# Optimization experiments

Measured on AMD Instinct MI355X. Metric: run time of the kernel, lower is better.

## Reference

```python
import jax, jax.numpy as jnp
import numpy as np

B, A, D, H = 2048, 32, 128, 256

def setup_inputs() -> dict:
    key = jax.random.key(0)
    ks = jax.random.split(key, 12)
    s = lambda fan_in: 1.0 / np.sqrt(fan_in)
    return {
        "obs": jax.random.normal(ks[0], (B, A, D), dtype=jnp.float32),
        "act": jax.random.normal(ks[1], (B, A, 8), dtype=jnp.float32),
        "enc_W": jax.random.uniform(ks[2], (H, D), jnp.float32, -s(D), s(D)),
        "enc_b": jax.random.uniform(ks[3], (H,), jnp.float32, -s(D), s(D)),
        "fobs_W": jax.random.uniform(ks[4], (H, H), jnp.float32, -s(H), s(H)),
        "fobs_b": jax.random.uniform(ks[5], (H,), jnp.float32, -s(H), s(H)),
        "W_ih": jax.random.uniform(ks[6], (3 * H, H), jnp.float32, -s(H), s(H)),
        "b_ih": jax.random.uniform(ks[7], (3 * H,), jnp.float32, -s(H), s(H)),
        "W_hh": jax.random.uniform(ks[8], (3 * H, H), jnp.float32, -s(H), s(H)),
        "b_hh": jax.random.uniform(ks[9], (3 * H,), jnp.float32, -s(H), s(H)),
        "dec_W": jax.random.uniform(ks[10], (1, H), jnp.float32, -s(H), s(H)),
        "dec_b": jax.random.uniform(ks[11], (1,), jnp.float32, -s(H), s(H)),
    }

def _gru_cell(x, h, W_ih, b_ih, W_hh, b_hh):
    # torch.nn.GRUCell: gates stacked as [reset, update, new]
    gi = x @ W_ih.T + b_ih          # [N, 3H]
    gh = h @ W_hh.T + b_hh          # [N, 3H]
    i_r, i_z, i_n = jnp.split(gi, 3, axis=-1)
    h_r, h_z, h_n = jnp.split(gh, 3, axis=-1)
    r = jax.nn.sigmoid(i_r + h_r)
    z = jax.nn.sigmoid(i_z + h_z)
    n = jnp.tanh(i_n + r * h_n)
    return (1.0 - z) * n + z * h

def reference(obs, act, enc_W, enc_b, fobs_W, fobs_b, W_ih, b_ih, W_hh, b_hh, dec_W, dec_b):
    b, a, d = obs.shape
    x = obs.reshape(b * a, d)                         # [B*A, D]
    e = jax.nn.relu(x @ enc_W.T + enc_b)              # encoder + ReLU
    h = e @ fobs_W.T + fobs_b                         # h_out
    # k = 0: comm input is zeros
    h = _gru_cell(jnp.zeros_like(h), h, W_ih, b_ih, W_hh, b_hh)
    # k = 1: masked mean over other agents == (sum_j h_j - h_i) / n_agents
    hA = h.reshape(b, a, -1)                          # [B, A, H]
    c = (hA.sum(axis=1, keepdims=True) - hA) / a      # [B, A, H]
    h = _gru_cell(c.reshape(b * a, -1), h, W_ih, b_ih, W_hh, b_hh)
    return (h @ dec_W.T + dec_b).reshape(b, a, -1)    # [B, A, 1]
```

## Files before the change

### kernel.cpp

```cpp
#include <hip/hip_runtime.h>
#include <hip/hip_fp16.h>


#define NB   2048
#define NA   32
#define DIN  128
#define HID  256
#define SA   264
#define MROWS 64

typedef _Float16 half8  __attribute__((ext_vector_type(8)));
typedef float    float4v __attribute__((ext_vector_type(4)));

#define ENC_OFF    0
#define FOBS_OFF   32768
#define WIH_OFF    98304
#define WHH_OFF    294912
#define PREP_TOTAL 491520

__global__ void prep_weights(const float* __restrict__ encW, const float* __restrict__ fobsW,
                             const float* __restrict__ wih,  const float* __restrict__ whh,
                             _Float16* __restrict__ prep) {
    int F = blockIdx.x * 256 + threadIdx.x;
    if (F >= PREP_TOTAL) return;
    const float* src; int K, NT, local = F;
    if (F < FOBS_OFF)     { src = encW;  K = 128; NT = 16; }
    else if (F < WIH_OFF) { src = fobsW; K = 256; NT = 16; local = F - FOBS_OFF; }
    else if (F < WHH_OFF) { src = wih;   K = 256; NT = 48; local = F - WIH_OFF; }
    else                  { src = whh;   K = 256; NT = 48; local = F - WHH_OFF; }
    int j    = local & 7;
    int lane = (local >> 3) & 63;
    int t    = local >> 9;
    int nt   = t % NT;
    int ks   = t / NT;
    int col  = nt * 16 + (lane & 15);
    int k    = ks * 32 + ((lane >> 4) << 3) + j;
    prep[F] = (_Float16)src[col * K + k];
}

__device__ __forceinline__ float sigmoid_f(float x) {
    x = fminf(fmaxf(x, -30.f), 30.f);
    return 1.f / (1.f + __expf(-x));
}
__device__ __forceinline__ float tanh_f(float x) {
    x = fminf(fmaxf(x, -15.f), 15.f);
    float e = __expf(-2.f * x);
    return (1.f - e) / (1.f + e);
}

__device__ __forceinline__ half8 ldB(const _Float16* __restrict__ prepm, int NT, int nt, int ks,
                                     const float* __restrict__ raw, int K, int use_prep, int lane) {
    if (use_prep)
        return *(const half8*)(prepm + (((ks * NT + nt) * 64 + lane) << 3));
    half8 b;
    int l16 = lane & 15, kq = (lane >> 4) << 3;
    #pragma unroll
    for (int j = 0; j < 8; j++)
        b[j] = (_Float16)raw[(nt * 16 + l16) * K + ks * 32 + kq + j];
    return b;
}

template<int KSTEPS>
__device__ __forceinline__ void gemm_col16(const _Float16* __restrict__ Abuf,
        const _Float16* __restrict__ prepm, int NT, int nt,
        const float* __restrict__ raw, int K, int use_prep,
        int lane, float4v acc[4])
{
    const int l16 = lane & 15;
    const int kq  = (lane >> 4) << 3;
    #pragma unroll 2
    for (int ks = 0; ks < KSTEPS; ks++) {
        int kbase = ks * 32 + kq;
        half8 Af[4];
        #pragma unroll
        for (int mt = 0; mt < 4; mt++)
            Af[mt] = *(const half8*)(Abuf + (mt * 16 + l16) * SA + kbase);
        half8 b0 = ldB(prepm, NT, nt, ks, raw, K, use_prep, lane);
        #pragma unroll
        for (int mt = 0; mt < 4; mt++)
            acc[mt] = __builtin_amdgcn_mfma_f32_16x16x32_f16(Af[mt], b0, acc[mt], 0, 0, 0);
    }
}

__global__ __launch_bounds__(1024) void commnet_fused(
    const float* __restrict__ obs, const _Float16* __restrict__ prep,
    const float* __restrict__ enc_b, const float* __restrict__ fobs_b,
    const float* __restrict__ b_ih, const float* __restrict__ b_hh,
    const float* __restrict__ dec_W, const float* __restrict__ dec_b,
    float* __restrict__ out,
    const float* __restrict__ encW, const float* __restrict__ fobsW,
    const float* __restrict__ wih, const float* __restrict__ whh,
    int use_prep)
{
    const int b    = blockIdx.x;
    const int tid  = threadIdx.x;
    const int lane = tid & 63;
    const int w    = tid >> 6;
    const int l16  = lane & 15;
    const int quad = lane >> 4;
    const int kq   = quad << 3;
    const int col  = w * 16 + l16;

    __shared__ __align__(16) _Float16 sA[2][MROWS * SA];
    __shared__ __align__(16) float S[2][HID];
    __shared__ float Srow[MROWS];

    {
        const float* obsb = obs + (size_t)b * MROWS * DIN;
        int r   = tid >> 4;
        int off = (tid & 15) << 3;
        const float* src = obsb + r * DIN + off;
        float4v v0 = *(const float4v*)(src);
        float4v v1 = *(const float4v*)(src + 4);
        half8 hv;
        hv[0] = (_Float16)v0[0]; hv[1] = (_Float16)v0[1];
        hv[2] = (_Float16)v0[2]; hv[3] = (_Float16)v0[3];
        hv[4] = (_Float16)v1[0]; hv[5] = (_Float16)v1[1];
        hv[6] = (_Float16)v1[2]; hv[7] = (_Float16)v1[3];
        *(half8*)(&sA[0][r * SA + off]) = hv;
    }
    __syncthreads();

    float4v acc[4];

    {
        float4v z = {0.f, 0.f, 0.f, 0.f};
        acc[0] = z; acc[1] = z; acc[2] = z; acc[3] = z;
        gemm_col16<4>(&sA[0][0], prep + ENC_OFF, 16, w, encW, DIN, use_prep, lane, acc);
        float bb = enc_b[col];
        #pragma unroll
        for (int mt = 0; mt < 4; mt++)
            #pragma unroll
            for (int r = 0; r < 4; r++) {
                int row = mt * 16 + quad * 4 + r;
                sA[1][row * SA + col] = (_Float16)fmaxf(acc[mt][r] + bb, 0.f);
            }
    }
    __syncthreads();

    {
        float4v z = {0.f, 0.f, 0.f, 0.f};
        acc[0] = z; acc[1] = z; acc[2] = z; acc[3] = z;
        gemm_col16<8>(&sA[1][0], prep + FOBS_OFF, 16, w, fobsW, HID, use_prep, lane, acc);
        float bb = fobs_b[col];
        #pragma unroll
        for (int mt = 0; mt < 4; mt++)
            #pragma unroll
            for (int r = 0; r < 4; r++) {
                int row = mt * 16 + quad * 4 + r;
                sA[0][row * SA + col] = (_Float16)(acc[mt][r] + bb);
            }
    }
    __syncthreads();

    {
        float4v aR[4], aZ[4], aN[4];
        float4v z = {0.f, 0.f, 0.f, 0.f};
        #pragma unroll
        for (int mt = 0; mt < 4; mt++) { aR[mt] = z; aZ[mt] = z; aN[mt] = z; }
        #pragma unroll 2
        for (int ks = 0; ks < 8; ks++) {
            const int kbase = ks * 32 + kq;
            half8 Af[4];
            #pragma unroll
            for (int mt = 0; mt < 4; mt++)
                Af[mt] = *(const half8*)(&sA[0][(mt * 16 + l16) * SA + kbase]);
            half8 bR = ldB(prep + WHH_OFF, 48,  0 + w, ks, whh, HID, use_prep, lane);
            half8 bZ = ldB(prep + WHH_OFF, 48, 16 + w, ks, whh, HID, use_prep, lane);
            half8 bN = ldB(prep + WHH_OFF, 48, 32 + w, ks, whh, HID, use_prep, lane);
            #pragma unroll
            for (int mt = 0; mt < 4; mt++)
                aR[mt] = __builtin_amdgcn_mfma_f32_16x16x32_f16(Af[mt], bR, aR[mt], 0, 0, 0);
            #pragma unroll
            for (int mt = 0; mt < 4; mt++)
                aZ[mt] = __builtin_amdgcn_mfma_f32_16x16x32_f16(Af[mt], bZ, aZ[mt], 0, 0, 0);
            #pragma unroll
            for (int mt = 0; mt < 4; mt++)
                aN[mt] = __builtin_amdgcn_mfma_f32_16x16x32_f16(Af[mt], bN, aN[mt], 0, 0, 0);
        }
        float biR = b_ih[col],       bhR = b_hh[col];
        float biZ = b_ih[256 + col], bhZ = b_hh[256 + col];
        float biN = b_ih[512 + col], bhN = b_hh[512 + col];
        float s0 = 0.f, s1 = 0.f;
        #pragma unroll
        for (int mt = 0; mt < 4; mt++) {
            float psum = 0.f;
            #pragma unroll
            for (int r = 0; r < 4; r++) {
                int row = mt * 16 + quad * 4 + r;
                float rg = sigmoid_f(biR + aR[mt][r] + bhR);
                float zg = sigmoid_f(biZ + aZ[mt][r] + bhZ);
                float ng = tanh_f(biN + rg * (aN[mt][r] + bhN));
                float hold = (float)sA[0][row * SA + col];
                float h1 = (1.f - zg) * ng + zg * hold;
                sA[1][row * SA + col] = (_Float16)h1;
                psum += h1;
            }
            if (mt < 2) s0 += psum; else s1 += psum;
        }
        s0 += __shfl_xor(s0, 16); s0 += __shfl_xor(s0, 32);
        s1 += __shfl_xor(s1, 16); s1 += __shfl_xor(s1, 32);
        if (lane < 16) { S[0][col] = s0; S[1][col] = s1; }
    }
    __syncthreads();

    {
        #pragma unroll
        for (int it = 0; it < 2; it++) {
            int i  = tid + it * 1024;
            int r  = i >> 5;
            int c8 = (i & 31) << 3;
            const float* Sp = &S[r >> 5][0];
            half8 hv = *(const half8*)(&sA[1][r * SA + c8]);
            float4v t0 = *(const float4v*)(Sp + c8);
            float4v t1 = *(const float4v*)(Sp + c8 + 4);
            half8 cv;
            cv[0] = (_Float16)((t0[0] - (float)hv[0]) * (1.f / 32.f));
            cv[1] = (_Float16)((t0[1] - (float)hv[1]) * (1.f / 32.f));
            cv[2] = (_Float16)((t0[2] - (float)hv[2]) * (1.f / 32.f));
            cv[3] = (_Float16)((t0[3] - (float)hv[3]) * (1.f / 32.f));
            cv[4] = (_Float16)((t1[0] - (float)hv[4]) * (1.f / 32.f));
            cv[5] = (_Float16)((t1[1] - (float)hv[5]) * (1.f / 32.f));
            cv[6] = (_Float16)((t1[2] - (float)hv[6]) * (1.f / 32.f));
            cv[7] = (_Float16)((t1[3] - (float)hv[7]) * (1.f / 32.f));
            *(half8*)(&sA[0][r * SA + c8]) = cv;
        }
        if (tid < MROWS) Srow[tid] = 0.f;
    }
    __syncthreads();

    {
        float4v aR[4], aZ[4], aNi[4], aNh[4];
        float4v z = {0.f, 0.f, 0.f, 0.f};
        #pragma unroll
        for (int mt = 0; mt < 4; mt++) { aR[mt] = z; aZ[mt] = z; aNi[mt] = z; aNh[mt] = z; }
        #pragma unroll 2
        for (int ks = 0; ks < 8; ks++) {
            const int kbase = ks * 32 + kq;
            {
                half8 Cf[4];
                #pragma unroll
                for (int mt = 0; mt < 4; mt++)
                    Cf[mt] = *(const half8*)(&sA[0][(mt * 16 + l16) * SA + kbase]);
                half8 bR = ldB(prep + WIH_OFF, 48,  0 + w, ks, wih, HID, use_prep, lane);
                half8 bZ = ldB(prep + WIH_OFF, 48, 16 + w, ks, wih, HID, use_prep, lane);
                half8 bN = ldB(prep + WIH_OFF, 48, 32 + w, ks, wih, HID, use_prep, lane);
                #pragma unroll
                for (int mt = 0; mt < 4; mt++)
                    aR[mt]  = __builtin_amdgcn_mfma_f32_16x16x32_f16(Cf[mt], bR, aR[mt], 0, 0, 0);
                #pragma unroll
                for (int mt = 0; mt < 4; mt++)
                    aZ[mt]  = __builtin_amdgcn_mfma_f32_16x16x32_f16(Cf[mt], bZ, aZ[mt], 0, 0, 0);
                #pragma unroll
                for (int mt = 0; mt < 4; mt++)
                    aNi[mt] = __builtin_amdgcn_mfma_f32_16x16x32_f16(Cf[mt], bN, aNi[mt], 0, 0, 0);
            }
            {
                half8 Hf[4];
                #pragma unroll
                for (int mt = 0; mt < 4; mt++)
                    Hf[mt] = *(const half8*)(&sA[1][(mt * 16 + l16) * SA + kbase]);
                half8 bR = ldB(prep + WHH_OFF, 48,  0 + w, ks, whh, HID, use_prep, lane);
                half8 bZ = ldB(prep + WHH_OFF, 48, 16 + w, ks, whh, HID, use_prep, lane);
                half8 bN = ldB(prep + WHH_OFF, 48, 32 + w, ks, whh, HID, use_prep, lane);
                #pragma unroll
                for (int mt = 0; mt < 4; mt++)
                    aR[mt]  = __builtin_amdgcn_mfma_f32_16x16x32_f16(Hf[mt], bR, aR[mt], 0, 0, 0);
                #pragma unroll
                for (int mt = 0; mt < 4; mt++)
                    aZ[mt]  = __builtin_amdgcn_mfma_f32_16x16x32_f16(Hf[mt], bZ, aZ[mt], 0, 0, 0);
                #pragma unroll
                for (int mt = 0; mt < 4; mt++)
                    aNh[mt] = __builtin_amdgcn_mfma_f32_16x16x32_f16(Hf[mt], bN, aNh[mt], 0, 0, 0);
            }
        }

        float biR = b_ih[col],       bhR = b_hh[col];
        float biZ = b_ih[256 + col], bhZ = b_hh[256 + col];
        float biN = b_ih[512 + col], bhN = b_hh[512 + col];
        float dw  = dec_W[col];
        float p[4][4];
        #pragma unroll
        for (int mt = 0; mt < 4; mt++)
            #pragma unroll
            for (int r = 0; r < 4; r++) {
                int row = mt * 16 + quad * 4 + r;
                float rg = sigmoid_f(aR[mt][r] + biR + bhR);
                float zg = sigmoid_f(aZ[mt][r] + biZ + bhZ);
                float ng = tanh_f((aNi[mt][r] + biN) + rg * (aNh[mt][r] + bhN));
                float h1v = (float)sA[1][row * SA + col];
                float h2 = (1.f - zg) * ng + zg * h1v;
                p[mt][r] = h2 * dw;
            }
        #pragma unroll
        for (int m = 1; m <= 8; m <<= 1) {
            #pragma unroll
            for (int mt = 0; mt < 4; mt++)
                #pragma unroll
                for (int r = 0; r < 4; r++)
                    p[mt][r] += __shfl_xor(p[mt][r], m);
        }
        if (l16 == 0) {
            #pragma unroll
            for (int mt = 0; mt < 4; mt++)
                #pragma unroll
                for (int r = 0; r < 4; r++)
                    atomicAdd(&Srow[mt * 16 + quad * 4 + r], p[mt][r]);
        }
    }
    __syncthreads();
    if (tid < MROWS) out[(size_t)b * MROWS + tid] = Srow[tid] + dec_b[0];
}

extern "C" void kernel_launch(void* const* d_in, const int* in_sizes, int n_in,
                              void* d_out, int out_size, void* d_ws, size_t ws_size,
                              hipStream_t stream) {
    const float* obs   = (const float*)d_in[0];
    const float* encW  = (const float*)d_in[2];
    const float* encb  = (const float*)d_in[3];
    const float* fobsW = (const float*)d_in[4];
    const float* fobsb = (const float*)d_in[5];
    const float* wih   = (const float*)d_in[6];
    const float* bih   = (const float*)d_in[7];
    const float* whh   = (const float*)d_in[8];
    const float* bhh   = (const float*)d_in[9];
    const float* decW  = (const float*)d_in[10];
    const float* decb  = (const float*)d_in[11];
    float* out = (float*)d_out;

    _Float16* prep = (_Float16*)d_ws;
    int use_prep = (ws_size >= (size_t)PREP_TOTAL * sizeof(_Float16)) ? 1 : 0;
    if (use_prep) {
        prep_weights<<<(PREP_TOTAL + 255) / 256, 256, 0, stream>>>(encW, fobsW, wih, whh, prep);
    }
    commnet_fused<<<NB / 2, 1024, 0, stream>>>(obs, prep, encb, fobsb, bih, bhh, decW, decb, out,
                                               encW, fobsW, wih, whh, use_prep);
}
```

Measured before the change: 247.8 us.

## Split GRU gate GEMMs into row halves and keep h_out in registers

The two GRU stages now run as two passes over 32-row halves, so each pass holds 6–8 accumulator vectors instead of 12–16. This is meant to cut register pressure under the 1024-thread launch bound and avoid spills. The fobs output is kept in fp32 registers (hacc) and used as the GRU's previous hidden state, replacing the reload of its fp16 copy from shared memory. The sigmoid/tanh clamps are dropped and tanh uses a cheaper formula; the trade-offs are weight loads issued twice per stage and possible inf/NaN edge cases without the clamps.

After: 236.6 us. -4.5%, faster.

```diff
diff --git a/kernel.cpp b/kernel.cpp
--- a/kernel.cpp
+++ b/kernel.cpp
@@ -39,13 +39,10 @@
 }
 
 __device__ __forceinline__ float sigmoid_f(float x) {
-    x = fminf(fmaxf(x, -30.f), 30.f);
     return 1.f / (1.f + __expf(-x));
 }
 __device__ __forceinline__ float tanh_f(float x) {
-    x = fminf(fmaxf(x, -15.f), 15.f);
-    float e = __expf(-2.f * x);
-    return (1.f - e) / (1.f + e);
+    return 1.f - 2.f / (__expf(2.f * x) + 1.f);
 }
 
 __device__ __forceinline__ half8 ldB(const _Float16* __restrict__ prepm, int NT, int nt, int ks,
@@ -58,28 +55,6 @@
     for (int j = 0; j < 8; j++)
         b[j] = (_Float16)raw[(nt * 16 + l16) * K + ks * 32 + kq + j];
     return b;
-}
-
-template<int KSTEPS>
-__device__ __forceinline__ void gemm_col16(const _Float16* __restrict__ Abuf,
-        const _Float16* __restrict__ prepm, int NT, int nt,
-        const float* __restrict__ raw, int K, int use_prep,
-        int lane, float4v acc[4])
-{
-    const int l16 = lane & 15;
-    const int kq  = (lane >> 4) << 3;
-    #pragma unroll 2
-    for (int ks = 0; ks < KSTEPS; ks++) {
-        int kbase = ks * 32 + kq;
-        half8 Af[4];
-        #pragma unroll
-        for (int mt = 0; mt < 4; mt++)
-            Af[mt] = *(const half8*)(Abuf + (mt * 16 + l16) * SA + kbase);
-        half8 b0 = ldB(prepm, NT, nt, ks, raw, K, use_prep, lane);
-        #pragma unroll
-        for (int mt = 0; mt < 4; mt++)
-            acc[mt] = __builtin_amdgcn_mfma_f32_16x16x32_f16(Af[mt], b0, acc[mt], 0, 0, 0);
-    }
 }
 
 __global__ __launch_bounds__(1024) void commnet_fused(
@@ -95,11 +70,11 @@
     const int b    = blockIdx.x;
     const int tid  = threadIdx.x;
     const int lane = tid & 63;
-    const int w    = tid >> 6;
+    const int nt   = tid >> 6;
     const int l16  = lane & 15;
     const int quad = lane >> 4;
     const int kq   = quad << 3;
-    const int col  = w * 16 + l16;
+    const int col  = nt * 16 + l16;
 
     __shared__ __align__(16) _Float16 sA[2][MROWS * SA];
     __shared__ __align__(16) float S[2][HID];
@@ -121,12 +96,22 @@
     }
     __syncthreads();
 
-    float4v acc[4];
-
     {
+        float4v acc[4];
         float4v z = {0.f, 0.f, 0.f, 0.f};
         acc[0] = z; acc[1] = z; acc[2] = z; acc[3] = z;
-        gemm_col16<4>(&sA[0][0], prep + ENC_OFF, 16, w, encW, DIN, use_prep, lane, acc);
+        #pragma unroll
+        for (int ks = 0; ks < 4; ks++) {
+            int kbase = ks * 32 + kq;
+            half8 Af[4];
+            #pragma unroll
+            for (int mt = 0; mt < 4; mt++)
+                Af[mt] = *(const half8*)(&sA[0][(mt * 16 + l16) * SA + kbase]);
+            half8 b0 = ldB(prep + ENC_OFF, 16, nt, ks, encW, DIN, use_prep, lane);
+            #pragma unroll
+            for (int mt = 0; mt < 4; mt++)
+                acc[mt] = __builtin_amdgcn_mfma_f32_16x16x32_f16(Af[mt], b0, acc[mt], 0, 0, 0);
+        }
         float bb = enc_b[col];
         #pragma unroll
         for (int mt = 0; mt < 4; mt++)
@@ -138,69 +123,76 @@
     }
     __syncthreads();
 
+    float4v hacc[4];
     {
         float4v z = {0.f, 0.f, 0.f, 0.f};
-        acc[0] = z; acc[1] = z; acc[2] = z; acc[3] = z;
-        gemm_col16<8>(&sA[1][0], prep + FOBS_OFF, 16, w, fobsW, HID, use_prep, lane, acc);
+        hacc[0] = z; hacc[1] = z; hacc[2] = z; hacc[3] = z;
+        #pragma unroll 2
+        for (int ks = 0; ks < 8; ks++) {
+            int kbase = ks * 32 + kq;
+            half8 Af[4];
+            #pragma unroll
+            for (int mt = 0; mt < 4; mt++)
+                Af[mt] = *(const half8*)(&sA[1][(mt * 16 + l16) * SA + kbase]);
+            half8 b0 = ldB(prep + FOBS_OFF, 16, nt, ks, fobsW, HID, use_prep, lane);
+            #pragma unroll
+            for (int mt = 0; mt < 4; mt++)
+                hacc[mt] = __builtin_amdgcn_mfma_f32_16x16x32_f16(Af[mt], b0, hacc[mt], 0, 0, 0);
+        }
         float bb = fobs_b[col];
         #pragma unroll
         for (int mt = 0; mt < 4; mt++)
             #pragma unroll
             for (int r = 0; r < 4; r++) {
                 int row = mt * 16 + quad * 4 + r;
-                sA[0][row * SA + col] = (_Float16)(acc[mt][r] + bb);
-            }
-    }
-    __syncthreads();
-
-    {
-        float4v aR[4], aZ[4], aN[4];
+                float h = hacc[mt][r] + bb;
+                hacc[mt][r] = h;
+                sA[0][row * SA + col] = (_Float16)h;
+            }
+    }
+    __syncthreads();
+
+    #pragma unroll 1
+    for (int half = 0; half < 2; half++) {
+        const int rb = half * 32;
+        float4v aR[2], aZ[2], aN[2];
         float4v z = {0.f, 0.f, 0.f, 0.f};
-        #pragma unroll
-        for (int mt = 0; mt < 4; mt++) { aR[mt] = z; aZ[mt] = z; aN[mt] = z; }
+        aR[0] = z; aR[1] = z; aZ[0] = z; aZ[1] = z; aN[0] = z; aN[1] = z;
         #pragma unroll 2
         for (int ks = 0; ks < 8; ks++) {
             const int kbase = ks * 32 + kq;
-            half8 Af[4];
-            #pragma unroll
-            for (int mt = 0; mt < 4; mt++)
-                Af[mt] = *(const half8*)(&sA[0][(mt * 16 + l16) * SA + kbase]);
-            half8 bR = ldB(prep + WHH_OFF, 48,  0 + w, ks, whh, HID, use_prep, lane);
-            half8 bZ = ldB(prep + WHH_OFF, 48, 16 + w, ks, whh, HID, use_prep, lane);
-            half8 bN = ldB(prep + WHH_OFF, 48, 32 + w, ks, whh, HID, use_prep, lane);
-            #pragma unroll
-            for (int mt = 0; mt < 4; mt++)
-                aR[mt] = __builtin_amdgcn_mfma_f32_16x16x32_f16(Af[mt], bR, aR[mt], 0, 0, 0);
-            #pragma unroll
-            for (int mt = 0; mt < 4; mt++)
-                aZ[mt] = __builtin_amdgcn_mfma_f32_16x16x32_f16(Af[mt], bZ, aZ[mt], 0, 0, 0);
-            #pragma unroll
-            for (int mt = 0; mt < 4; mt++)
-                aN[mt] = __builtin_amdgcn_mfma_f32_16x16x32_f16(Af[mt], bN, aN[mt], 0, 0, 0);
+            half8 A0 = *(const half8*)(&sA[0][(rb + l16) * SA + kbase]);
+            half8 A1 = *(const half8*)(&sA[0][(rb + 16 + l16) * SA + kbase]);
+            half8 bR = ldB(prep + WHH_OFF, 48,  0 + nt, ks, whh, HID, use_prep, lane);
+            half8 bZ = ldB(prep + WHH_OFF, 48, 16 + nt, ks, whh, HID, use_prep, lane);
+            half8 bN = ldB(prep + WHH_OFF, 48, 32 + nt, ks, whh, HID, use_prep, lane);
+            aR[0] = __builtin_amdgcn_mfma_f32_16x16x32_f16(A0, bR, aR[0], 0, 0, 0);
+            aR[1] = __builtin_amdgcn_mfma_f32_16x16x32_f16(A1, bR, aR[1], 0, 0, 0);
+            aZ[0] = __builtin_amdgcn_mfma_f32_16x16x32_f16(A0, bZ, aZ[0], 0, 0, 0);
+            aZ[1] = __builtin_amdgcn_mfma_f32_16x16x32_f16(A1, bZ, aZ[1], 0, 0, 0);
+            aN[0] = __builtin_amdgcn_mfma_f32_16x16x32_f16(A0, bN, aN[0], 0, 0, 0);
+            aN[1] = __builtin_amdgcn_mfma_f32_16x16x32_f16(A1, bN, aN[1], 0, 0, 0);
         }
         float biR = b_ih[col],       bhR = b_hh[col];
         float biZ = b_ih[256 + col], bhZ = b_hh[256 + col];
         float biN = b_ih[512 + col], bhN = b_hh[512 + col];
-        float s0 = 0.f, s1 = 0.f;
-        #pragma unroll
-        for (int mt = 0; mt < 4; mt++) {
-            float psum = 0.f;
+        float psum = 0.f;
+        #pragma unroll
+        for (int mt = 0; mt < 2; mt++)
             #pragma unroll
             for (int r = 0; r < 4; r++) {
-                int row = mt * 16 + quad * 4 + r;
+                int row = rb + mt * 16 + quad * 4 + r;
                 float rg = sigmoid_f(biR + aR[mt][r] + bhR);
                 float zg = sigmoid_f(biZ + aZ[mt][r] + bhZ);
                 float ng = tanh_f(biN + rg * (aN[mt][r] + bhN));
-                float hold = (float)sA[0][row * SA + col];
+                float hold = hacc[half * 2 + mt][r];
                 float h1 = (1.f - zg) * ng + zg * hold;
                 sA[1][row * SA + col] = (_Float16)h1;
                 psum += h1;
             }
-            if (mt < 2) s0 += psum; else s1 += psum;
-        }
-        s0 += __shfl_xor(s0, 16); s0 += __shfl_xor(s0, 32);
-        s1 += __shfl_xor(s1, 16); s1 += __shfl_xor(s1, 32);
-        if (lane < 16) { S[0][col] = s0; S[1][col] = s1; }
+        psum += __shfl_xor(psum, 16);
+        psum += __shfl_xor(psum, 32);
+        if (lane < 16) S[half][nt * 16 + lane] = psum;
     }
     __syncthreads();
 
@@ -229,49 +221,41 @@
     }
     __syncthreads();
 
-    {
-        float4v aR[4], aZ[4], aNi[4], aNh[4];
+    #pragma unroll 1
+    for (int half = 0; half < 2; half++) {
+        const int rb = half * 32;
+        float4v aR[2], aZ[2], aNi[2], aNh[2];
         float4v z = {0.f, 0.f, 0.f, 0.f};
-        #pragma unroll
-        for (int mt = 0; mt < 4; mt++) { aR[mt] = z; aZ[mt] = z; aNi[mt] = z; aNh[mt] = z; }
-        #pragma unroll 2
+        aR[0] = z; aR[1] = z; aZ[0] = z; aZ[1] = z;
+        aNi[0] = z; aNi[1] = z; aNh[0] = z; aNh[1] = z;
+        #pragma unroll 1
         for (int ks = 0; ks < 8; ks++) {
             const int kbase = ks * 32 + kq;
             {
-                half8 Cf[4];
-                #pragma unroll
-                for (int mt = 0; mt < 4; mt++)
-                    Cf[mt] = *(const half8*)(&sA[0][(mt * 16 + l16) * SA + kbase]);
-                half8 bR = ldB(prep + WIH_OFF, 48,  0 + w, ks, wih, HID, use_prep, lane);
-                half8 bZ = ldB(prep + WIH_OFF, 48, 16 + w, ks, wih, HID, use_prep, lane);
-                half8 bN = ldB(prep + WIH_OFF, 48, 32 + w, ks, wih, HID, use_prep, lane);
-                #pragma unroll
-                for (int mt = 0; mt < 4; mt++)
-                    aR[mt]  = __builtin_amdgcn_mfma_f32_16x16x32_f16(Cf[mt], bR, aR[mt], 0, 0, 0);
-                #pragma unroll
-                for (int mt = 0; mt < 4; mt++)
-                    aZ[mt]  = __builtin_amdgcn_mfma_f32_16x16x32_f16(Cf[mt], bZ, aZ[mt], 0, 0, 0);
-                #pragma unroll
-                for (int mt = 0; mt < 4; mt++)
-                    aNi[mt] = __builtin_amdgcn_mfma_f32_16x16x32_f16(Cf[mt], bN, aNi[mt], 0, 0, 0);
+                half8 C0 = *(const half8*)(&sA[0][(rb + l16) * SA + kbase]);
+                half8 C1 = *(const half8*)(&sA[0][(rb + 16 + l16) * SA + kbase]);
+                half8 bR = ldB(prep + WIH_OFF, 48,  0 + nt, ks, wih, HID, use_prep, lane);
+                half8 bZ = ldB(prep + WIH_OFF, 48, 16 + nt, ks, wih, HID, use_prep, lane);
+                half8 bN = ldB(prep + WIH_OFF, 48, 32 + nt, ks, wih, HID, use_prep, lane);
+                aR[0]  = __builtin_amdgcn_mfma_f32_16x16x32_f16(C0, bR, aR[0], 0, 0, 0);
+                aR[1]  = __builtin_amdgcn_mfma_f32_16x16x32_f16(C1, bR, aR[1], 0, 0, 0);
+                aZ[0]  = __builtin_amdgcn_mfma_f32_16x16x32_f16(C0, bZ, aZ[0], 0, 0, 0);
+                aZ[1]  = __builtin_amdgcn_mfma_f32_16x16x32_f16(C1, bZ, aZ[1], 0, 0, 0);
+                aNi[0] = __builtin_amdgcn_mfma_f32_16x16x32_f16(C0, bN, aNi[0], 0, 0, 0);
+                aNi[1] = __builtin_amdgcn_mfma_f32_16x16x32_f16(C1, bN, aNi[1], 0, 0, 0);
             }
             {
-                half8 Hf[4];
-                #pragma unroll
-                for (int mt = 0; mt < 4; mt++)
-                    Hf[mt] = *(const half8*)(&sA[1][(mt * 16 + l16) * SA + kbase]);
-                half8 bR = ldB(prep + WHH_OFF, 48,  0 + w, ks, whh, HID, use_prep, lane);
-                half8 bZ = ldB(prep + WHH_OFF, 48, 16 + w, ks, whh, HID, use_prep, lane);
-                half8 bN = ldB(prep + WHH_OFF, 48, 32 + w, ks, whh, HID, use_prep, lane);
-                #pragma unroll
-                for (int mt = 0; mt < 4; mt++)
-                    aR[mt]  = __builtin_amdgcn_mfma_f32_16x16x32_f16(Hf[mt], bR, aR[mt], 0, 0, 0);
-                #pragma unroll
-                for (int mt = 0; mt < 4; mt++)
-                    aZ[mt]  = __builtin_amdgcn_mfma_f32_16x16x32_f16(Hf[mt], bZ, aZ[mt], 0, 0, 0);
-                #pragma unroll
-                for (int mt = 0; mt < 4; mt++)
-                    aNh[mt] = __builtin_amdgcn_mfma_f32_16x16x32_f16(Hf[mt], bN, aNh[mt], 0, 0, 0);
+                half8 H0 = *(const half8*)(&sA[1][(rb + l16) * SA + kbase]);
+                half8 H1 = *(const half8*)(&sA[1][(rb + 16 + l16) * SA + kbase]);
+                half8 bR = ldB(prep + WHH_OFF, 48,  0 + nt, ks, whh, HID, use_prep, lane);
+                half8 bZ = ldB(prep + WHH_OFF, 48, 16 + nt, ks, whh, HID, use_prep, lane);
+                half8 bN = ldB(prep + WHH_OFF, 48, 32 + nt, ks, whh, HID, use_prep, lane);
+                aR[0]  = __builtin_amdgcn_mfma_f32_16x16x32_f16(H0, bR, aR[0], 0, 0, 0);
+                aR[1]  = __builtin_amdgcn_mfma_f32_16x16x32_f16(H1, bR, aR[1], 0, 0, 0);
+                aZ[0]  = __builtin_amdgcn_mfma_f32_16x16x32_f16(H0, bZ, aZ[0], 0, 0, 0);
+                aZ[1]  = __builtin_amdgcn_mfma_f32_16x16x32_f16(H1, bZ, aZ[1], 0, 0, 0);
+                aNh[0] = __builtin_amdgcn_mfma_f32_16x16x32_f16(H0, bN, aNh[0], 0, 0, 0);
+                aNh[1] = __builtin_amdgcn_mfma_f32_16x16x32_f16(H1, bN, aNh[1], 0, 0, 0);
             }
         }
 
@@ -279,12 +263,12 @@
         float biZ = b_ih[256 + col], bhZ = b_hh[256 + col];
         float biN = b_ih[512 + col], bhN = b_hh[512 + col];
         float dw  = dec_W[col];
-        float p[4][4];
-        #pragma unroll
-        for (int mt = 0; mt < 4; mt++)
+        float p[2][4];
+        #pragma unroll
+        for (int mt = 0; mt < 2; mt++)
             #pragma unroll
             for (int r = 0; r < 4; r++) {
-                int row = mt * 16 + quad * 4 + r;
+                int row = rb + mt * 16 + quad * 4 + r;
                 float rg = sigmoid_f(aR[mt][r] + biR + bhR);
                 float zg = sigmoid_f(aZ[mt][r] + biZ + bhZ);
                 float ng = tanh_f((aNi[mt][r] + biN) + rg * (aNh[mt][r] + bhN));
@@ -295,17 +279,17 @@
         #pragma unroll
         for (int m = 1; m <= 8; m <<= 1) {
             #pragma unroll
-            for (int mt = 0; mt < 4; mt++)
+            for (int mt = 0; mt < 2; mt++)
                 #pragma unroll
                 for (int r = 0; r < 4; r++)
                     p[mt][r] += __shfl_xor(p[mt][r], m);
         }
         if (l16 == 0) {
             #pragma unroll
-            for (int mt = 0; mt < 4; mt++)
+            for (int mt = 0; mt < 2; mt++)
                 #pragma unroll
                 for (int r = 0; r < 4; r++)
-                    atomicAdd(&Srow[mt * 16 + quad * 4 + r], p[mt][r]);
+                    atomicAdd(&Srow[rb + mt * 16 + quad * 4 + r], p[mt][r]);
         }
     }
     __syncthreads();
```
